# Optimization experiments

Measured on AMD Instinct MI355X. Metric: run time of the kernel, lower is better.

## Reference

```python
import jax, jax.numpy as jnp
import numpy as np

N_NODES = 100000
N_EDGES = 150000
D_IN = 512
D_HID = 512
N_GRAPHS = 64


def setup_inputs() -> dict:
    key = jax.random.key(0)
    ks = jax.random.split(key, 12)
    x = jax.random.normal(ks[0], (N_NODES, D_IN), dtype=jnp.float32)
    edge_index = jax.random.randint(ks[1], (2, N_EDGES), 0, N_NODES, dtype=jnp.int64)
    batch = jnp.sort(jax.random.randint(ks[2], (N_NODES,), 0, N_GRAPHS, dtype=jnp.int64))
    s1 = 1.0 / np.sqrt(D_IN)
    s2 = 1.0 / np.sqrt(D_HID)
    # GINConv layer 1: MLP([D_IN, D_HID, D_HID])
    W1a = jax.random.uniform(ks[3], (D_IN, D_HID), jnp.float32, -s1, s1)
    b1a = jax.random.uniform(ks[4], (D_HID,), jnp.float32, -s1, s1)
    W1b = jax.random.uniform(ks[5], (D_HID, D_HID), jnp.float32, -s2, s2)
    b1b = jax.random.uniform(ks[6], (D_HID,), jnp.float32, -s2, s2)
    # GINConv layer 2 (out_channels=1): MLP([D_HID, 1, 1])
    W2a = jax.random.uniform(ks[7], (D_HID, 1), jnp.float32, -s2, s2)
    b2a = jax.random.uniform(ks[8], (1,), jnp.float32, -s2, s2)
    W2b = jax.random.uniform(ks[9], (1, 1), jnp.float32, -1.0, 1.0)
    b2b = jax.random.uniform(ks[10], (1,), jnp.float32, -1.0, 1.0)
    return {"x": x, "edge_index": edge_index, "batch": batch,
            "W1a": W1a, "b1a": b1a, "W1b": W1b, "b1b": b1b,
            "W2a": W2a, "b2a": b2a, "W2b": W2b, "b2b": b2b}


def _gin_conv(h, src, dst, Wa, ba, Wb, bb):
    # sum-aggregate neighbor features, add (1+eps)*x with eps=0, then MLP
    agg = jax.ops.segment_sum(h[src], dst, num_segments=N_NODES)  # [N, d]
    z = agg + h
    z = jnp.maximum(jnp.dot(z, Wa) + ba, 0.0)  # Linear -> ReLU
    return jnp.dot(z, Wb) + bb                  # Linear (plain last)


def reference(x, edge_index, batch, W1a, b1a, W1b, b1b, W2a, b2a, W2b, b2b):
    src, dst = edge_index[0], edge_index[1]
    h = _gin_conv(x, src, dst, W1a, b1a, W1b, b1b)
    h = jnp.maximum(h, 0.0)  # inter-layer activation (not applied after last layer)
    h = _gin_conv(h, src, dst, W2a, b2a, W2b, b2b)  # [N, 1]
    # global mean pool over graph assignment
    sums = jax.ops.segment_sum(h, batch, num_segments=N_GRAPHS)  # [G, 1]
    cnt = jax.ops.segment_sum(jnp.ones((N_NODES, 1), h.dtype), batch, num_segments=N_GRAPHS)
    return sums / jnp.maximum(cnt, 1.0)
```

## Files before the change

### kernel.cpp

```cpp
#include <hip/hip_runtime.h>
#include <hip/hip_bf16.h>

#define N_NODES_C 100000
#define N_EDGES_C 150000
#define DC 512
#define NG 64

typedef float f32x4 __attribute__((ext_vector_type(4)));
typedef short s16x8 __attribute__((ext_vector_type(8)));
typedef unsigned int u32;

__device__ __forceinline__ short f2bf(float f) {
    union { float f; unsigned u; } c; c.f = f;
    unsigned r = c.u + 0x7fffu + ((c.u >> 16) & 1u);
    return (short)(r >> 16);
}
__device__ __forceinline__ float bf2f(short v) {
    union { unsigned u; float f; } c;
    c.u = ((unsigned)(unsigned short)v) << 16;
    return c.f;
}

__device__ __forceinline__ void gload16(const void* g, void* l) {
    __builtin_amdgcn_global_load_lds((const __attribute__((address_space(1))) u32*)g,
                                     (__attribute__((address_space(3))) u32*)l,
                                     16, 0, 0);
}


__global__ void zero_k(float* s, float* aggs, int* cnt, float* gsum, float* gcnt) {
    int i = blockIdx.x * 256 + threadIdx.x;
    if (i < N_NODES_C) { s[i] = 0.f; aggs[i] = 0.f; cnt[i] = 0; }
    if (i < NG) { gsum[i] = 0.f; gcnt[i] = 0.f; }
}

__global__ void transpose_w2(const float* __restrict__ in0, const float* __restrict__ in1,
                             short* __restrict__ out0, short* __restrict__ out1) {
    __shared__ float tile[32][33];
    const float* in = blockIdx.z ? in1 : in0;
    short* out = blockIdx.z ? out1 : out0;
    int tx = threadIdx.x & 31;
    int ty = threadIdx.x >> 5;
    int k0 = blockIdx.y * 32;
    int n0 = blockIdx.x * 32;
#pragma unroll
    for (int i = 0; i < 4; ++i)
        tile[ty + i * 8][tx] = in[(size_t)(k0 + ty + i * 8) * DC + n0 + tx];
    __syncthreads();
#pragma unroll
    for (int i = 0; i < 4; ++i)
        out[(size_t)(n0 + ty + i * 8) * DC + k0 + tx] = f2bf(tile[tx][ty + i * 8]);
}


__global__ void hist_k(const int* __restrict__ ei, int* __restrict__ cnt) {
    int e = blockIdx.x * 256 + threadIdx.x;
    if (e < N_EDGES_C) atomicAdd(&cnt[ei[N_EDGES_C + e]], 1);
}

__global__ void scan1_k(const int* __restrict__ cnt, int* __restrict__ off,
                        int* __restrict__ bsum) {
    __shared__ int sh[1024];
    int tid = threadIdx.x;
    int i = blockIdx.x * 1024 + tid;
    int v = (i < N_NODES_C) ? cnt[i] : 0;
    sh[tid] = v;
    __syncthreads();
    for (int d = 1; d < 1024; d <<= 1) {
        int t = (tid >= d) ? sh[tid - d] : 0;
        __syncthreads();
        sh[tid] += t;
        __syncthreads();
    }
    if (i < N_NODES_C) off[i] = sh[tid] - v;
    if (tid == 1023) bsum[blockIdx.x] = sh[1023];
}

#define NSCAN_BLK 98

__global__ void scan2_k(int* __restrict__ bsum) {
    __shared__ int sh[128];
    int tid = threadIdx.x;
    int v = (tid < NSCAN_BLK) ? bsum[tid] : 0;
    sh[tid] = v;
    __syncthreads();
    for (int d = 1; d < 128; d <<= 1) {
        int t = (tid >= d) ? sh[tid - d] : 0;
        __syncthreads();
        sh[tid] += t;
        __syncthreads();
    }
    if (tid < NSCAN_BLK) bsum[tid] = sh[tid] - v;
}

__global__ void scan3_k(int* __restrict__ off, const int* __restrict__ bsum) {
    int i = blockIdx.x * 1024 + threadIdx.x;
    if (i < N_NODES_C) off[i] += bsum[blockIdx.x];
}

__global__ void place_k(const int* __restrict__ ei, int* __restrict__ off,
                        int* __restrict__ ssrc) {
    int e = blockIdx.x * 256 + threadIdx.x;
    if (e < N_EDGES_C) {
        int d = ei[N_EDGES_C + e];
        int p = atomicAdd(&off[d], 1);
        ssrc[p] = ei[e];
    }
}

__global__ void gather_relu_k(const short* __restrict__ y, const int* __restrict__ off,
                              const int* __restrict__ ssrc, const float* __restrict__ b1a,
                              short* __restrict__ z1) {
    int node = blockIdx.x * 4 + (threadIdx.x >> 6);
    if (node >= N_NODES_C) return;
    int t = threadIdx.x & 63;
    const int col = t * 8;
    int beg = (node == 0) ? 0 : off[node - 1];
    int end = off[node];
    s16x8 own = *(const s16x8*)(y + (size_t)node * DC + col);
    float acc[8];
#pragma unroll
    for (int q = 0; q < 8; ++q) acc[q] = bf2f(own[q]);
    int j = beg;
    for (; j + 2 <= end; j += 2) {
        int s0 = ssrc[j];
        int s1 = ssrc[j + 1];
        s16x8 r0 = *(const s16x8*)(y + (size_t)s0 * DC + col);
        s16x8 r1 = *(const s16x8*)(y + (size_t)s1 * DC + col);
#pragma unroll
        for (int q = 0; q < 8; ++q) acc[q] += bf2f(r0[q]) + bf2f(r1[q]);
    }
    if (j < end) {
        int s0 = ssrc[j];
        s16x8 r0 = *(const s16x8*)(y + (size_t)s0 * DC + col);
#pragma unroll
        for (int q = 0; q < 8; ++q) acc[q] += bf2f(r0[q]);
    }
    f32x4 bv0 = *(const f32x4*)(b1a + col);
    f32x4 bv1 = *(const f32x4*)(b1a + col + 4);
    s16x8 o;
    o[0] = f2bf(fmaxf(acc[0] + bv0.x, 0.f));
    o[1] = f2bf(fmaxf(acc[1] + bv0.y, 0.f));
    o[2] = f2bf(fmaxf(acc[2] + bv0.z, 0.f));
    o[3] = f2bf(fmaxf(acc[3] + bv0.w, 0.f));
    o[4] = f2bf(fmaxf(acc[4] + bv1.x, 0.f));
    o[5] = f2bf(fmaxf(acc[5] + bv1.y, 0.f));
    o[6] = f2bf(fmaxf(acc[6] + bv1.z, 0.f));
    o[7] = f2bf(fmaxf(acc[7] + bv1.w, 0.f));
    *(s16x8*)(z1 + (size_t)node * DC + col) = o;
}


__global__ void edge_scalar(const int* __restrict__ ei, const float* __restrict__ s,
                            float* __restrict__ aggs) {
    int e = blockIdx.x * 256 + threadIdx.x;
    if (e < N_EDGES_C) atomicAdd(&aggs[ei[N_EDGES_C + e]], s[ei[e]]);
}

__global__ void node_pool(const float* __restrict__ s, const float* __restrict__ aggs,
                          const int* __restrict__ batch, const float* __restrict__ b2a,
                          float* __restrict__ gsum, float* __restrict__ gcnt) {
    __shared__ float ls[NG], lc[NG];
    int t = threadIdx.x;
    if (t < NG) { ls[t] = 0.f; lc[t] = 0.f; }
    __syncthreads();
    int i = blockIdx.x * 256 + t;
    if (i < N_NODES_C) {
        float z2 = fmaxf(aggs[i] + s[i] + b2a[0], 0.0f);
        int g = batch[i];
        atomicAdd(&ls[g], z2);
        atomicAdd(&lc[g], 1.0f);
    }
    __syncthreads();
    if (t < NG && lc[t] != 0.f) {
        atomicAdd(&gsum[t], ls[t]);
        atomicAdd(&gcnt[t], lc[t]);
    }
}

__global__ void finalize_k(const float* gsum, const float* gcnt, const float* w2b,
                           const float* b2b, float* out) {
    int g = threadIdx.x;
    if (g < NG) {
        float c = fmaxf(gcnt[g], 1.0f);
        out[g] = gsum[g] / c * w2b[0] + b2b[0];
    }
}

#define BM 128
#define BN 128
#define BK 32
#define NKT (DC / BK)
#define NWG 3128
#define WPX 391

__global__ __launch_bounds__(256, 3) void gemm0_k(const float* __restrict__ Ap,
                                                  const short* __restrict__ Bt,
                                                  short* __restrict__ Cout) {
    __shared__ alignas(16) short As[BM * BK];
    __shared__ alignas(16) short Bs[BN * BK];

    const int tid = threadIdx.x;
    const int bid = blockIdx.x;
    const int lin = (bid & 7) * WPX + (bid >> 3);
    const int brow = (lin >> 2) * BM;
    const int bcol = (lin & 3) * BN;

    const int w    = tid >> 6;
    const int lane = tid & 63;
    const int wr   = (w >> 1) * 64;
    const int wc   = (w & 1) * 64;
    const int lr   = lane & 15;
    const int lg   = lane >> 4;
    const int lswz = (lr >> 1) & 3;

    f32x4 acc[4][4] = {};

    const int srow = lane >> 2;
    const int scol = (((lane & 3) ^ ((srow >> 1) & 3)) * 8);

    const short* bg0 = Bt + (size_t)(bcol + w * 32 + srow) * DC + scol;
    const short* bg1 = bg0 + (size_t)16 * DC;
    short* bl0 = &Bs[(w * 32) * BK];
    short* bl1 = &Bs[(w * 32 + 16) * BK];

    const int rAl = tid >> 1;
    int r = brow + rAl;
    if (r >= N_NODES_C) r = N_NODES_C - 1;
    const float* axsrc = Ap + (size_t)r * DC + (tid & 1) * 16;
    const int rswz = (rAl >> 1) & 3;
    const int awoff0 = rAl * BK + ((((tid & 1) * 2 + 0) ^ rswz) * 8);
    const int awoff1 = rAl * BK + ((((tid & 1) * 2 + 1) ^ rswz) * 8);

    f32x4 areg[4];
#pragma unroll
    for (int q = 0; q < 4; ++q) areg[q] = *(const f32x4*)(axsrc + q * 4);

    for (int kt = 0; kt < NKT; ++kt) {
        const int k0 = kt * BK;
        __syncthreads();
        s16x8 c0, c1;
        c0[0] = f2bf(areg[0].x); c0[1] = f2bf(areg[0].y);
        c0[2] = f2bf(areg[0].z); c0[3] = f2bf(areg[0].w);
        c0[4] = f2bf(areg[1].x); c0[5] = f2bf(areg[1].y);
        c0[6] = f2bf(areg[1].z); c0[7] = f2bf(areg[1].w);
        c1[0] = f2bf(areg[2].x); c1[1] = f2bf(areg[2].y);
        c1[2] = f2bf(areg[2].z); c1[3] = f2bf(areg[2].w);
        c1[4] = f2bf(areg[3].x); c1[5] = f2bf(areg[3].y);
        c1[6] = f2bf(areg[3].z); c1[7] = f2bf(areg[3].w);
        *(s16x8*)&As[awoff0] = c0;
        *(s16x8*)&As[awoff1] = c1;
        gload16(bg0 + k0, bl0);
        gload16(bg1 + k0, bl1);
        __syncthreads();

        if (kt + 1 < NKT) {
#pragma unroll
            for (int q = 0; q < 4; ++q)
                areg[q] = *(const f32x4*)(axsrc + (kt + 1) * BK + q * 4);
        }

        s16x8 af[4], bfr[4];
#pragma unroll
        for (int mi = 0; mi < 4; ++mi)
            af[mi] = *(const s16x8*)&As[(wr + mi * 16 + lr) * BK + ((lg ^ lswz) * 8)];
#pragma unroll
        for (int ni = 0; ni < 4; ++ni)
            bfr[ni] = *(const s16x8*)&Bs[(wc + ni * 16 + lr) * BK + ((lg ^ lswz) * 8)];
        __builtin_amdgcn_s_setprio(1);
#pragma unroll
        for (int mi = 0; mi < 4; ++mi)
#pragma unroll
            for (int ni = 0; ni < 4; ++ni)
                acc[mi][ni] = __builtin_amdgcn_mfma_f32_16x16x32_bf16(af[mi], bfr[ni],
                                                                      acc[mi][ni], 0, 0, 0);
        __builtin_amdgcn_s_setprio(0);
    }

    const int rb = brow + wr + lg * 4;
    const int cb = bcol + wc + lr;
#pragma unroll
    for (int mi = 0; mi < 4; ++mi) {
#pragma unroll
        for (int rr = 0; rr < 4; ++rr) {
            int row = rb + mi * 16 + rr;
            if (row < N_NODES_C) {
#pragma unroll
                for (int ni = 0; ni < 4; ++ni)
                    Cout[(size_t)row * DC + cb + ni * 16] = f2bf(acc[mi][ni][rr]);
            }
        }
    }
}

#define G2_BM 256
#define G2_NWG 1564

__global__ __launch_bounds__(512, 2) void gemm1_k(const short* __restrict__ A,
                                                  const short* __restrict__ Bt,
                                                  const float* __restrict__ bias,
                                                  const float* __restrict__ w2a,
                                                  float* __restrict__ s_out) {
    __shared__ alignas(16) short As[G2_BM * BK];
    __shared__ alignas(16) short Bs[BN * BK];

    const int tid = threadIdx.x;
    const int bid = blockIdx.x;
    const int q = G2_NWG / 8, rr8 = G2_NWG % 8;
    const int xcd = bid & 7;
    const int lin = (xcd < rr8 ? xcd * (q + 1) : rr8 * (q + 1) + (xcd - rr8) * q) + (bid >> 3);
    const int brow = (lin >> 2) * G2_BM;
    const int bcol = (lin & 3) * BN;

    const int w    = tid >> 6;
    const int lane = tid & 63;
    const int wm   = w >> 1;
    const int wn   = w & 1;
    const int lr   = lane & 15;
    const int lg   = lane >> 4;
    const int lswz = (lr >> 1) & 3;

    f32x4 acc[4][4] = {};

    const int srow = lane >> 2;
    const int scol = (((lane & 3) ^ ((srow >> 1) & 3)) * 8);

    int ar0 = brow + w * 32 + srow;
    int ar1 = ar0 + 16;
    if (ar0 >= N_NODES_C) ar0 = N_NODES_C - 1;
    if (ar1 >= N_NODES_C) ar1 = N_NODES_C - 1;
    const short* ag0 = A + (size_t)ar0 * DC + scol;
    const short* ag1 = A + (size_t)ar1 * DC + scol;
    short* al0 = &As[(w * 32) * BK];
    short* al1 = &As[(w * 32 + 16) * BK];
    const short* bg = Bt + (size_t)(bcol + w * 16 + srow) * DC + scol;
    short* bl = &Bs[(w * 16) * BK];

    for (int kt = 0; kt < NKT; ++kt) {
        const int k0 = kt * BK;
        __syncthreads();
        gload16(ag0 + k0, al0);
        gload16(ag1 + k0, al1);
        gload16(bg + k0, bl);
        __syncthreads();

        s16x8 af[4], bfr[4];
#pragma unroll
        for (int mi = 0; mi < 4; ++mi)
            af[mi] = *(const s16x8*)&As[(wm * 64 + mi * 16 + lr) * BK + ((lg ^ lswz) * 8)];
#pragma unroll
        for (int ni = 0; ni < 4; ++ni)
            bfr[ni] = *(const s16x8*)&Bs[(wn * 64 + ni * 16 + lr) * BK + ((lg ^ lswz) * 8)];
        __builtin_amdgcn_s_setprio(1);
#pragma unroll
        for (int mi = 0; mi < 4; ++mi)
#pragma unroll
            for (int ni = 0; ni < 4; ++ni)
                acc[mi][ni] = __builtin_amdgcn_mfma_f32_16x16x32_bf16(af[mi], bfr[ni],
                                                                      acc[mi][ni], 0, 0, 0);
        __builtin_amdgcn_s_setprio(0);
    }

    const int rb = brow + wm * 64 + lg * 4;
    const int cb = bcol + wn * 64 + lr;

    float bv[4], wv[4];
#pragma unroll
    for (int ni = 0; ni < 4; ++ni) {
        bv[ni] = bias[cb + ni * 16];
        wv[ni] = w2a[cb + ni * 16];
    }
#pragma unroll
    for (int mi = 0; mi < 4; ++mi) {
#pragma unroll
        for (int rr = 0; rr < 4; ++rr) {
            float sum = 0.f;
#pragma unroll
            for (int ni = 0; ni < 4; ++ni) {
                float v = fmaxf(acc[mi][ni][rr] + bv[ni], 0.0f);
                sum += v * wv[ni];
            }
#pragma unroll
            for (int off = 1; off < 16; off <<= 1) sum += __shfl_xor(sum, off, 64);
            int row = rb + mi * 16 + rr;
            if (lr == 0 && row < N_NODES_C) atomicAdd(&s_out[row], sum);
        }
    }
}


extern "C" void kernel_launch(void* const* d_in, const int* in_sizes, int n_in,
                              void* d_out, int out_size, void* d_ws, size_t ws_size,
                              hipStream_t stream) {
    const float* x     = (const float*)d_in[0];
    const int*   ei    = (const int*)d_in[1];
    const int*   batch = (const int*)d_in[2];
    const float* W1a   = (const float*)d_in[3];
    const float* b1a   = (const float*)d_in[4];
    const float* W1b   = (const float*)d_in[5];
    const float* b1b   = (const float*)d_in[6];
    const float* W2a   = (const float*)d_in[7];
    const float* b2a   = (const float*)d_in[8];
    const float* W2b   = (const float*)d_in[9];
    const float* b2b   = (const float*)d_in[10];
    float* out = (float*)d_out;

    char* w = (char*)d_ws;
    short* z1   = (short*)(w);
    short* y    = (short*)(w + 102400000);
    short* WT1  = (short*)(w + 204800000);
    short* WT2  = (short*)(w + 205324288);
    float* sbuf = (float*)(w + 205848576);
    float* aggs = (float*)(w + 206248576);
    int*   cnt  = (int*)  (w + 206648576);
    int*   offb = (int*)  (w + 207048576);
    int*   ssrc = (int*)  (w + 207448576);
    int*   bsum = (int*)  (w + 208048576);
    float* gsum = (float*)(w + 208049088);
    float* gcnt = (float*)(w + 208049344);

    zero_k<<<391, 256, 0, stream>>>(sbuf, aggs, cnt, gsum, gcnt);
    transpose_w2<<<dim3(16, 16, 2), 256, 0, stream>>>(W1a, W1b, WT1, WT2);

    hist_k<<<586, 256, 0, stream>>>(ei, cnt);
    scan1_k<<<NSCAN_BLK, 1024, 0, stream>>>(cnt, offb, bsum);
    scan2_k<<<1, 128, 0, stream>>>(bsum);
    scan3_k<<<NSCAN_BLK, 1024, 0, stream>>>(offb, bsum);
    place_k<<<586, 256, 0, stream>>>(ei, offb, ssrc);

    gemm0_k<<<NWG, 256, 0, stream>>>(x, WT1, y);
    gather_relu_k<<<25000, 256, 0, stream>>>(y, offb, ssrc, b1a, z1);
    gemm1_k<<<G2_NWG, 512, 0, stream>>>(z1, WT2, b1b, W2a, sbuf);

    edge_scalar<<<586, 256, 0, stream>>>(ei, sbuf, aggs);
    node_pool<<<391, 256, 0, stream>>>(sbuf, aggs, batch, b2a, gsum, gcnt);
    finalize_k<<<1, 64, 0, stream>>>(gsum, gcnt, W2b, b2b, out);
}
```

Before: 299.5 us.

## Double-buffer LDS in both GEMMs, retile gemm1, replace zero kernel with memsets

Both GEMM kernels now use two LDS stages, so the next k-tile is prefetched while MFMAs run on the current one. This drops one barrier per iteration. gemm1 moves from 256-row tiles with 512 threads to 128-row tiles with 256 threads and higher occupancy, reusing gemm0's XCD block mapping. The zeroing kernel is replaced by hipMemsetAsync calls. Doubling LDS raises shared memory per block, which may limit occupancy.

Result: no change. 299.3 us (-0.1%).

```diff
diff --git a/kernel.cpp b/kernel.cpp
--- a/kernel.cpp
+++ b/kernel.cpp
@@ -27,12 +27,6 @@
                                      16, 0, 0);
 }
 
-
-__global__ void zero_k(float* s, float* aggs, int* cnt, float* gsum, float* gcnt) {
-    int i = blockIdx.x * 256 + threadIdx.x;
-    if (i < N_NODES_C) { s[i] = 0.f; aggs[i] = 0.f; cnt[i] = 0; }
-    if (i < NG) { gsum[i] = 0.f; gcnt[i] = 0.f; }
-}
 
 __global__ void transpose_w2(const float* __restrict__ in0, const float* __restrict__ in1,
                              short* __restrict__ out0, short* __restrict__ out1) {
@@ -197,8 +191,8 @@
 __global__ __launch_bounds__(256, 3) void gemm0_k(const float* __restrict__ Ap,
                                                   const short* __restrict__ Bt,
                                                   short* __restrict__ Cout) {
-    __shared__ alignas(16) short As[BM * BK];
-    __shared__ alignas(16) short Bs[BN * BK];
+    __shared__ alignas(16) short As[2][BM * BK];
+    __shared__ alignas(16) short Bs[2][BN * BK];
 
     const int tid = threadIdx.x;
     const int bid = blockIdx.x;
@@ -221,8 +215,6 @@
 
     const short* bg0 = Bt + (size_t)(bcol + w * 32 + srow) * DC + scol;
     const short* bg1 = bg0 + (size_t)16 * DC;
-    short* bl0 = &Bs[(w * 32) * BK];
-    short* bl1 = &Bs[(w * 32 + 16) * BK];
 
     const int rAl = tid >> 1;
     int r = brow + rAl;
@@ -233,40 +225,47 @@
     const int awoff1 = rAl * BK + ((((tid & 1) * 2 + 1) ^ rswz) * 8);
 
     f32x4 areg[4];
+
+#define CVT_WRITE_A(buf)                                         \
+    do {                                                         \
+        s16x8 c0, c1;                                            \
+        c0[0] = f2bf(areg[0].x); c0[1] = f2bf(areg[0].y);        \
+        c0[2] = f2bf(areg[0].z); c0[3] = f2bf(areg[0].w);        \
+        c0[4] = f2bf(areg[1].x); c0[5] = f2bf(areg[1].y);        \
+        c0[6] = f2bf(areg[1].z); c0[7] = f2bf(areg[1].w);        \
+        c1[0] = f2bf(areg[2].x); c1[1] = f2bf(areg[2].y);        \
+        c1[2] = f2bf(areg[2].z); c1[3] = f2bf(areg[2].w);        \
+        c1[4] = f2bf(areg[3].x); c1[5] = f2bf(areg[3].y);        \
+        c1[6] = f2bf(areg[3].z); c1[7] = f2bf(areg[3].w);        \
+        *(s16x8*)&As[buf][awoff0] = c0;                          \
+        *(s16x8*)&As[buf][awoff1] = c1;                          \
+    } while (0)
+
 #pragma unroll
     for (int q = 0; q < 4; ++q) areg[q] = *(const f32x4*)(axsrc + q * 4);
+    CVT_WRITE_A(0);
+    gload16(bg0, &Bs[0][(w * 32) * BK]);
+    gload16(bg1, &Bs[0][(w * 32 + 16) * BK]);
+    __syncthreads();
 
     for (int kt = 0; kt < NKT; ++kt) {
-        const int k0 = kt * BK;
-        __syncthreads();
-        s16x8 c0, c1;
-        c0[0] = f2bf(areg[0].x); c0[1] = f2bf(areg[0].y);
-        c0[2] = f2bf(areg[0].z); c0[3] = f2bf(areg[0].w);
-        c0[4] = f2bf(areg[1].x); c0[5] = f2bf(areg[1].y);
-        c0[6] = f2bf(areg[1].z); c0[7] = f2bf(areg[1].w);
-        c1[0] = f2bf(areg[2].x); c1[1] = f2bf(areg[2].y);
-        c1[2] = f2bf(areg[2].z); c1[3] = f2bf(areg[2].w);
-        c1[4] = f2bf(areg[3].x); c1[5] = f2bf(areg[3].y);
-        c1[6] = f2bf(areg[3].z); c1[7] = f2bf(areg[3].w);
-        *(s16x8*)&As[awoff0] = c0;
-        *(s16x8*)&As[awoff1] = c1;
-        gload16(bg0 + k0, bl0);
-        gload16(bg1 + k0, bl1);
-        __syncthreads();
-
+        const int cur = kt & 1;
         if (kt + 1 < NKT) {
+            const int k1 = (kt + 1) * BK;
 #pragma unroll
             for (int q = 0; q < 4; ++q)
-                areg[q] = *(const f32x4*)(axsrc + (kt + 1) * BK + q * 4);
+                areg[q] = *(const f32x4*)(axsrc + k1 + q * 4);
+            gload16(bg0 + k1, &Bs[cur ^ 1][(w * 32) * BK]);
+            gload16(bg1 + k1, &Bs[cur ^ 1][(w * 32 + 16) * BK]);
         }
 
         s16x8 af[4], bfr[4];
 #pragma unroll
         for (int mi = 0; mi < 4; ++mi)
-            af[mi] = *(const s16x8*)&As[(wr + mi * 16 + lr) * BK + ((lg ^ lswz) * 8)];
+            af[mi] = *(const s16x8*)&As[cur][(wr + mi * 16 + lr) * BK + ((lg ^ lswz) * 8)];
 #pragma unroll
         for (int ni = 0; ni < 4; ++ni)
-            bfr[ni] = *(const s16x8*)&Bs[(wc + ni * 16 + lr) * BK + ((lg ^ lswz) * 8)];
+            bfr[ni] = *(const s16x8*)&Bs[cur][(wc + ni * 16 + lr) * BK + ((lg ^ lswz) * 8)];
         __builtin_amdgcn_s_setprio(1);
 #pragma unroll
         for (int mi = 0; mi < 4; ++mi)
@@ -275,7 +274,11 @@
                 acc[mi][ni] = __builtin_amdgcn_mfma_f32_16x16x32_bf16(af[mi], bfr[ni],
                                                                       acc[mi][ni], 0, 0, 0);
         __builtin_amdgcn_s_setprio(0);
-    }
+
+        if (kt + 1 < NKT) CVT_WRITE_A(cur ^ 1);
+        __syncthreads();
+    }
+#undef CVT_WRITE_A
 
     const int rb = brow + wr + lg * 4;
     const int cb = bcol + wc + lr;
@@ -293,29 +296,24 @@
     }
 }
 
-#define G2_BM 256
-#define G2_NWG 1564
-
-__global__ __launch_bounds__(512, 2) void gemm1_k(const short* __restrict__ A,
+__global__ __launch_bounds__(256, 4) void gemm1_k(const short* __restrict__ A,
                                                   const short* __restrict__ Bt,
                                                   const float* __restrict__ bias,
                                                   const float* __restrict__ w2a,
                                                   float* __restrict__ s_out) {
-    __shared__ alignas(16) short As[G2_BM * BK];
-    __shared__ alignas(16) short Bs[BN * BK];
+    __shared__ alignas(16) short As[2][BM * BK];
+    __shared__ alignas(16) short Bs[2][BN * BK];
 
     const int tid = threadIdx.x;
     const int bid = blockIdx.x;
-    const int q = G2_NWG / 8, rr8 = G2_NWG % 8;
-    const int xcd = bid & 7;
-    const int lin = (xcd < rr8 ? xcd * (q + 1) : rr8 * (q + 1) + (xcd - rr8) * q) + (bid >> 3);
-    const int brow = (lin >> 2) * G2_BM;
+    const int lin = (bid & 7) * WPX + (bid >> 3);
+    const int brow = (lin >> 2) * BM;
     const int bcol = (lin & 3) * BN;
 
     const int w    = tid >> 6;
     const int lane = tid & 63;
-    const int wm   = w >> 1;
-    const int wn   = w & 1;
+    const int wr   = (w >> 1) * 64;
+    const int wc   = (w & 1) * 64;
     const int lr   = lane & 15;
     const int lg   = lane >> 4;
     const int lswz = (lr >> 1) & 3;
@@ -331,26 +329,31 @@
     if (ar1 >= N_NODES_C) ar1 = N_NODES_C - 1;
     const short* ag0 = A + (size_t)ar0 * DC + scol;
     const short* ag1 = A + (size_t)ar1 * DC + scol;
-    short* al0 = &As[(w * 32) * BK];
-    short* al1 = &As[(w * 32 + 16) * BK];
-    const short* bg = Bt + (size_t)(bcol + w * 16 + srow) * DC + scol;
-    short* bl = &Bs[(w * 16) * BK];
+    const short* bg0 = Bt + (size_t)(bcol + w * 32 + srow) * DC + scol;
+    const short* bg1 = bg0 + (size_t)16 * DC;
+
+#define STAGE1(k0, buf)                                  \
+    do {                                                 \
+        gload16(ag0 + (k0), &As[buf][(w * 32) * BK]);    \
+        gload16(ag1 + (k0), &As[buf][(w * 32 + 16) * BK]); \
+        gload16(bg0 + (k0), &Bs[buf][(w * 32) * BK]);    \
+        gload16(bg1 + (k0), &Bs[buf][(w * 32 + 16) * BK]); \
+    } while (0)
+
+    STAGE1(0, 0);
+    __syncthreads();
 
     for (int kt = 0; kt < NKT; ++kt) {
-        const int k0 = kt * BK;
-        __syncthreads();
-        gload16(ag0 + k0, al0);
-        gload16(ag1 + k0, al1);
-        gload16(bg + k0, bl);
-        __syncthreads();
+        const int cur = kt & 1;
+        if (kt + 1 < NKT) STAGE1((kt + 1) * BK, cur ^ 1);
 
         s16x8 af[4], bfr[4];
 #pragma unroll
         for (int mi = 0; mi < 4; ++mi)
-            af[mi] = *(const s16x8*)&As[(wm * 64 + mi * 16 + lr) * BK + ((lg ^ lswz) * 8)];
+            af[mi] = *(const s16x8*)&As[cur][(wr + mi * 16 + lr) * BK + ((lg ^ lswz) * 8)];
 #pragma unroll
         for (int ni = 0; ni < 4; ++ni)
-            bfr[ni] = *(const s16x8*)&Bs[(wn * 64 + ni * 16 + lr) * BK + ((lg ^ lswz) * 8)];
+            bfr[ni] = *(const s16x8*)&Bs[cur][(wc + ni * 16 + lr) * BK + ((lg ^ lswz) * 8)];
         __builtin_amdgcn_s_setprio(1);
 #pragma unroll
         for (int mi = 0; mi < 4; ++mi)
@@ -359,10 +362,12 @@
                 acc[mi][ni] = __builtin_amdgcn_mfma_f32_16x16x32_bf16(af[mi], bfr[ni],
                                                                       acc[mi][ni], 0, 0, 0);
         __builtin_amdgcn_s_setprio(0);
-    }
-
-    const int rb = brow + wm * 64 + lg * 4;
-    const int cb = bcol + wn * 64 + lr;
+        __syncthreads();
+    }
+#undef STAGE1
+
+    const int rb = brow + wr + lg * 4;
+    const int cb = bcol + wc + lr;
 
     float bv[4], wv[4];
 #pragma unroll
@@ -419,7 +424,8 @@
     float* gsum = (float*)(w + 208049088);
     float* gcnt = (float*)(w + 208049344);
 
-    zero_k<<<391, 256, 0, stream>>>(sbuf, aggs, cnt, gsum, gcnt);
+    hipMemsetAsync(sbuf, 0, 1200000, stream);
+    hipMemsetAsync(gsum, 0, 512, stream);
     transpose_w2<<<dim3(16, 16, 2), 256, 0, stream>>>(W1a, W1b, WT1, WT2);
 
     hist_k<<<586, 256, 0, stream>>>(ei, cnt);
@@ -430,7 +436,7 @@
 
     gemm0_k<<<NWG, 256, 0, stream>>>(x, WT1, y);
     gather_relu_k<<<25000, 256, 0, stream>>>(y, offb, ssrc, b1a, z1);
-    gemm1_k<<<G2_NWG, 512, 0, stream>>>(z1, WT2, b1b, W2a, sbuf);
+    gemm1_k<<<NWG, 256, 0, stream>>>(z1, WT2, b1b, W2a, sbuf);
 
     edge_scalar<<<586, 256, 0, stream>>>(ei, sbuf, aggs);
     node_pool<<<391, 256, 0, stream>>>(sbuf, aggs, batch, b2a, gsum, gcnt);
```

## Restructure second GEMM to keep full-K B panel in LDS and stream A directly

Applied to the files above, without the earlier changes.

Replaces the 256x128 tiled gemm1 kernel, which staged A and B through LDS in K-steps, with a 256x64 kernel. The new kernel loads the whole 64x512 B panel into swizzled LDS once, then reads A fragments straight from global memory into registers with no per-step barriers. This removes the per-K-tile synchronisation and LDS staging of A, but doubles the number of workgroups and re-reads A from global/L2 for each of the 8 column blocks. It also replaces the zeroing kernel with hipMemsetAsync calls over the contiguous workspace region.

Measured after the change: 365.9 us. +22.1%, slower.

```diff
diff --git a/kernel.cpp b/kernel.cpp
--- a/kernel.cpp
+++ b/kernel.cpp
@@ -27,12 +27,6 @@
                                      16, 0, 0);
 }
 
-
-__global__ void zero_k(float* s, float* aggs, int* cnt, float* gsum, float* gcnt) {
-    int i = blockIdx.x * 256 + threadIdx.x;
-    if (i < N_NODES_C) { s[i] = 0.f; aggs[i] = 0.f; cnt[i] = 0; }
-    if (i < NG) { gsum[i] = 0.f; gcnt[i] = 0.f; }
-}
 
 __global__ void transpose_w2(const float* __restrict__ in0, const float* __restrict__ in1,
                              short* __restrict__ out0, short* __restrict__ out1) {
@@ -293,64 +287,63 @@
     }
 }
 
-#define G2_BM 256
-#define G2_NWG 1564
-
-__global__ __launch_bounds__(512, 2) void gemm1_k(const short* __restrict__ A,
-                                                  const short* __restrict__ Bt,
-                                                  const float* __restrict__ bias,
-                                                  const float* __restrict__ w2a,
-                                                  float* __restrict__ s_out) {
-    __shared__ alignas(16) short As[G2_BM * BK];
-    __shared__ alignas(16) short Bs[BN * BK];
-
-    const int tid = threadIdx.x;
-    const int bid = blockIdx.x;
-    const int q = G2_NWG / 8, rr8 = G2_NWG % 8;
-    const int xcd = bid & 7;
-    const int lin = (xcd < rr8 ? xcd * (q + 1) : rr8 * (q + 1) + (xcd - rr8) * q) + (bid >> 3);
-    const int brow = (lin >> 2) * G2_BM;
-    const int bcol = (lin & 3) * BN;
+#define P_BM 256
+#define P_BN 64
+#define P_NWG 3128
+#define P_WPX 391
+
+__global__ __launch_bounds__(256, 2) void gemm1p_k(const short* __restrict__ A,
+                                                   const short* __restrict__ Bt,
+                                                   const float* __restrict__ bias,
+                                                   const float* __restrict__ w2a,
+                                                   float* __restrict__ s_out) {
+    __shared__ alignas(16) short Bs[P_BN * DC];
+
+    const int tid  = threadIdx.x;
+    const int bid  = blockIdx.x;
+    const int lin  = (bid & 7) * P_WPX + (bid >> 3);
+    const int brow = (lin >> 3) * P_BM;
+    const int bcol = (lin & 7) * P_BN;
 
     const int w    = tid >> 6;
     const int lane = tid & 63;
-    const int wm   = w >> 1;
-    const int wn   = w & 1;
     const int lr   = lane & 15;
     const int lg   = lane >> 4;
-    const int lswz = (lr >> 1) & 3;
+
+    {
+        const int r0 = tid >> 2;
+        const int q  = tid & 3;
+        const short* src = Bt + (size_t)(bcol + r0) * DC + q * 128;
+        short* dst = &Bs[r0 * DC];
+#pragma unroll
+        for (int c = 0; c < 16; ++c) {
+            const int gc = q * 16 + c;
+            *(s16x8*)&dst[(gc ^ (r0 & 7)) * 8] = *(const s16x8*)(src + c * 8);
+        }
+    }
+    __syncthreads();
 
     f32x4 acc[4][4] = {};
 
-    const int srow = lane >> 2;
-    const int scol = (((lane & 3) ^ ((srow >> 1) & 3)) * 8);
-
-    int ar0 = brow + w * 32 + srow;
-    int ar1 = ar0 + 16;
-    if (ar0 >= N_NODES_C) ar0 = N_NODES_C - 1;
-    if (ar1 >= N_NODES_C) ar1 = N_NODES_C - 1;
-    const short* ag0 = A + (size_t)ar0 * DC + scol;
-    const short* ag1 = A + (size_t)ar1 * DC + scol;
-    short* al0 = &As[(w * 32) * BK];
-    short* al1 = &As[(w * 32 + 16) * BK];
-    const short* bg = Bt + (size_t)(bcol + w * 16 + srow) * DC + scol;
-    short* bl = &Bs[(w * 16) * BK];
-
-    for (int kt = 0; kt < NKT; ++kt) {
-        const int k0 = kt * BK;
-        __syncthreads();
-        gload16(ag0 + k0, al0);
-        gload16(ag1 + k0, al1);
-        gload16(bg + k0, bl);
-        __syncthreads();
-
+    const short* ar[4];
+#pragma unroll
+    for (int mi = 0; mi < 4; ++mi) {
+        int r = brow + w * 64 + mi * 16 + lr;
+        if (r >= N_NODES_C) r = N_NODES_C - 1;
+        ar[mi] = A + (size_t)r * DC + lg * 8;
+    }
+
+#pragma unroll
+    for (int kt = 0; kt < 16; ++kt) {
         s16x8 af[4], bfr[4];
 #pragma unroll
         for (int mi = 0; mi < 4; ++mi)
-            af[mi] = *(const s16x8*)&As[(wm * 64 + mi * 16 + lr) * BK + ((lg ^ lswz) * 8)];
-#pragma unroll
-        for (int ni = 0; ni < 4; ++ni)
-            bfr[ni] = *(const s16x8*)&Bs[(wn * 64 + ni * 16 + lr) * BK + ((lg ^ lswz) * 8)];
+            af[mi] = *(const s16x8*)(ar[mi] + kt * 32);
+#pragma unroll
+        for (int ni = 0; ni < 4; ++ni) {
+            const int row = ni * 16 + lr;
+            bfr[ni] = *(const s16x8*)&Bs[row * DC + (((kt * 4 + lg) ^ (row & 7)) * 8)];
+        }
         __builtin_amdgcn_s_setprio(1);
 #pragma unroll
         for (int mi = 0; mi < 4; ++mi)
@@ -361,8 +354,8 @@
         __builtin_amdgcn_s_setprio(0);
     }
 
-    const int rb = brow + wm * 64 + lg * 4;
-    const int cb = bcol + wn * 64 + lr;
+    const int rb = brow + w * 64 + lg * 4;
+    const int cb = bcol + lr;
 
     float bv[4], wv[4];
 #pragma unroll
@@ -419,7 +412,8 @@
     float* gsum = (float*)(w + 208049088);
     float* gcnt = (float*)(w + 208049344);
 
-    zero_k<<<391, 256, 0, stream>>>(sbuf, aggs, cnt, gsum, gcnt);
+    hipMemsetAsync(sbuf, 0, 1200000, stream);
+    hipMemsetAsync(gsum, 0, 512, stream);
     transpose_w2<<<dim3(16, 16, 2), 256, 0, stream>>>(W1a, W1b, WT1, WT2);
 
     hist_k<<<586, 256, 0, stream>>>(ei, cnt);
@@ -430,7 +424,7 @@
 
     gemm0_k<<<NWG, 256, 0, stream>>>(x, WT1, y);
     gather_relu_k<<<25000, 256, 0, stream>>>(y, offb, ssrc, b1a, z1);
-    gemm1_k<<<G2_NWG, 512, 0, stream>>>(z1, WT2, b1b, W2a, sbuf);
+    gemm1p_k<<<P_NWG, 256, 0, stream>>>(z1, WT2, b1b, W2a, sbuf);
 
     edge_scalar<<<586, 256, 0, stream>>>(ei, sbuf, aggs);
     node_pool<<<391, 256, 0, stream>>>(sbuf, aggs, batch, b2a, gsum, gcnt);
```
